# Kernel optimization log

Measured on AMD Instinct MI355X. Metric: run time of the kernel, lower is better.

The kernel has to match this reference:

```python
import jax, jax.numpy as jnp
import numpy as np

T, B, D, HID, L = 256, 64, 1024, 1024, 2


def setup_inputs() -> dict:
    key = jax.random.key(0)
    k1, k2, k3 = jax.random.split(key, 3)
    X = jax.random.normal(k1, (T, B, D), dtype=jnp.float32)
    # Stacked gate weights in order (i, f, o, c); xavier-like scale.
    Wx = jax.random.normal(k2, (L, 4 * HID, D), dtype=jnp.float32) * 0.03
    Wh = jax.random.normal(k3, (L, 4 * HID, HID), dtype=jnp.float32) * 0.03
    # Combined bias (Linear bias + b_gate); forget-gate bias initialized to 1.
    b = jnp.zeros((L, 4 * HID), dtype=jnp.float32).at[:, HID:2 * HID].set(1.0)
    return {"X": X, "Wx": Wx, "Wh": Wh, "b": b}


def reference(X, Wx, Wh, b):
    num_layers, H4, _ = Wx.shape
    Hd = H4 // 4
    Bsz = X.shape[1]
    H0 = jnp.zeros((num_layers, Bsz, Hd), X.dtype)
    C0 = jnp.zeros((num_layers, Bsz, Hd), X.dtype)

    def step(carry, x_t):
        H, C = carry
        x = x_t
        Hn, Cn = [], []
        for l in range(num_layers):  # small fixed layer count
            # fused gate GEMM: [B, 4H]
            g = x @ Wx[l].T + H[l] @ Wh[l].T + b[l]
            i_g, f_g, o_g, c_g = jnp.split(g, 4, axis=-1)
            c = jax.nn.sigmoid(f_g) * C[l] + jax.nn.sigmoid(i_g) * jnp.tanh(c_g)
            h = jax.nn.sigmoid(o_g) * jnp.tanh(c)
            Hn.append(h)
            Cn.append(c)
            x = h  # dropout is identity in eval mode
        return (jnp.stack(Hn), jnp.stack(Cn)), x

    (Hf, Cf), outputs = jax.lax.scan(step, (H0, C0), X)
    return outputs, Hf, Cf
```

## Files before the change

kernel.cpp:

```cpp
#include <hip/hip_runtime.h>
#include <cstdint>
#include <cstddef>

typedef __attribute__((ext_vector_type(8))) short short8;
typedef __attribute__((ext_vector_type(4))) float floatx4;
typedef unsigned short u16;
typedef unsigned long long u64;

#define NSTEP 256

__device__ __forceinline__ unsigned f2b_rne(float x) {
  unsigned u = __builtin_bit_cast(unsigned, x);
  return (u + 0x7fffu + ((u >> 16) & 1u)) >> 16;
}
__device__ __forceinline__ float b2f(u16 b) {
  unsigned u = ((unsigned)b) << 16;
  return __builtin_bit_cast(float, u);
}
__device__ __forceinline__ float sigf(float x) {
  x = fminf(fmaxf(x, -30.f), 30.f);
  return __builtin_amdgcn_rcpf(1.f + __expf(-x));
}
__device__ __forceinline__ float tanhf_fast(float x) {
  x = fminf(fmaxf(x, -15.f), 15.f);
  float e = __expf(2.f * x);
  return (e - 1.f) * __builtin_amdgcn_rcpf(e + 1.f);
}

__device__ __forceinline__ unsigned ald(const unsigned* p) {
  return __hip_atomic_load(p, __ATOMIC_RELAXED, __HIP_MEMORY_SCOPE_AGENT);
}
__device__ __forceinline__ void ast(unsigned* p, unsigned v) {
  __hip_atomic_store(p, v, __ATOMIC_RELAXED, __HIP_MEMORY_SCOPE_AGENT);
}

__global__ void init_kernel(unsigned* h0, unsigned* h1) {
  int i = blockIdx.x * blockDim.x + threadIdx.x;
  if (i < 32768) { h0[i] = 0; h1[i] = 0; }
}

__global__ void init2_kernel(unsigned* fl) {
  int i = blockIdx.x * blockDim.x + threadIdx.x;
  if (i < 1536) fl[i] = 0;
}

__global__ void cast_kernel(const float* __restrict__ in, u16* __restrict__ out, int n4) {
  int i = blockIdx.x * blockDim.x + threadIdx.x;
  int stride = gridDim.x * blockDim.x;
  for (; i < n4; i += stride) {
    float4 v = ((const float4*)in)[i];
    unsigned lo = f2b_rne(v.x) | (f2b_rne(v.y) << 16);
    unsigned hi = f2b_rne(v.z) | (f2b_rne(v.w) << 16);
    ((uint2*)out)[i] = make_uint2(lo, hi);
  }
}

__global__ __launch_bounds__(256) void gemm_nt(
    const u16* __restrict__ A, const u16* __restrict__ B, u16* __restrict__ C) {
  __shared__ u16 As[128 * 32];
  __shared__ u16 Bs[128 * 32];
  const int bid = blockIdx.x;
  const int m_blk = (bid >> 5) << 7;
  const int n_blk = (bid & 31) << 7;
  const int tid = threadIdx.x;
  const int wv = tid >> 6, lane = tid & 63;
  const int q = lane >> 4, n16 = lane & 15;
  const int m0w = (wv >> 1) << 6, n0w = (wv & 1) << 6;

  const floatx4 vzero = {0.f, 0.f, 0.f, 0.f};
  floatx4 acc[4][4];
#pragma unroll
  for (int mt = 0; mt < 4; ++mt)
#pragma unroll
    for (int nt = 0; nt < 4; ++nt) acc[mt][nt] = vzero;

  for (int k0 = 0; k0 < 1024; k0 += 32) {
#pragma unroll
    for (int i = 0; i < 2; ++i) {
      int s = i * 256 + tid;
      int r = s >> 2, kk = (s & 3) << 3;
      int m = m_blk + r, k = k0 + kk;
      size_t a_off = (size_t)m * 1024 + k;
      size_t b_off = (size_t)(n_blk + r) * 1024 + k;
      __builtin_amdgcn_global_load_lds(
          (const __attribute__((address_space(1))) unsigned int*)(A + a_off),
          (__attribute__((address_space(3))) unsigned int*)(As + (size_t)(i * 256 + wv * 64) * 8),
          16, 0, 0);
      __builtin_amdgcn_global_load_lds(
          (const __attribute__((address_space(1))) unsigned int*)(B + b_off),
          (__attribute__((address_space(3))) unsigned int*)(Bs + (size_t)(i * 256 + wv * 64) * 8),
          16, 0, 0);
    }
    __syncthreads();
    short8 af[4], bf[4];
#pragma unroll
    for (int mt = 0; mt < 4; ++mt)
      af[mt] = *(const short8*)(As + (m0w + mt * 16 + n16) * 32 + q * 8);
#pragma unroll
    for (int nt = 0; nt < 4; ++nt)
      bf[nt] = *(const short8*)(Bs + (n0w + nt * 16 + n16) * 32 + q * 8);
#pragma unroll
    for (int mt = 0; mt < 4; ++mt)
#pragma unroll
      for (int nt = 0; nt < 4; ++nt)
        acc[mt][nt] = __builtin_amdgcn_mfma_f32_16x16x32_bf16(af[mt], bf[nt], acc[mt][nt], 0, 0, 0);
    __syncthreads();
  }
#pragma unroll
  for (int mt = 0; mt < 4; ++mt)
#pragma unroll
    for (int nt = 0; nt < 4; ++nt)
#pragma unroll
      for (int r = 0; r < 4; ++r) {
        int m = m_blk + m0w + mt * 16 + q * 4 + r;
        int n = n_blk + n0w + nt * 16 + n16;
        C[(size_t)m * 4096 + n] = (u16)f2b_rne(acc[mt][nt][r]);
      }
}

#define GEMM_Q(HROW, W)                                                        \
  {                                                                            \
    short8 a_[8][4];                                                           \
    _Pragma("unroll")                                                          \
    for (int c_ = 0; c_ < 8; ++c_) {                                           \
      int k_ = kq0 + c_ * 32 + q * 8;                                          \
      const unsigned* base_ = (HROW) + (k_ >> 4) * 512 + ((k_ & 15) >> 1);     \
      _Pragma("unroll")                                                        \
      for (int m_ = 0; m_ < 4; ++m_)                                           \
        a_[c_][m_] = *(const short8*)(base_ + (m_ * 16 + n16) * 8);            \
    }                                                                          \
    _Pragma("unroll")                                                          \
    for (int c_ = 0; c_ < 8; ++c_)                                             \
      _Pragma("unroll")                                                        \
      for (int m_ = 0; m_ < 4; ++m_)                                           \
        asm volatile("" : "+v"(a_[c_][m_]));                                   \
    _Pragma("unroll")                                                          \
    for (int c_ = 0; c_ < 8; ++c_)                                             \
      _Pragma("unroll")                                                        \
      for (int m_ = 0; m_ < 4; ++m_)                                           \
        _Pragma("unroll")                                                      \
        for (int g_ = 0; g_ < 4; ++g_)                                         \
          acc[m_][g_] = __builtin_amdgcn_mfma_f32_16x16x32_bf16(a_[c_][m_], (W)[g_][c_], acc[m_][g_], 0, 0, 0); \
  }

#define REDUCE_TOT()                                                           \
  _Pragma("unroll")                                                            \
  for (int m_ = 0; m_ < 4; ++m_) {                                             \
    if (m_ != wv) {                                                            \
      int slot_ = (m_ - (m_ > wv ? 1 : 0)) * 4;                                \
      _Pragma("unroll")                                                        \
      for (int g_ = 0; g_ < 4; ++g_)                                           \
        *(floatx4*)&red[wv][slot_ + g_][lane * 4] = acc[m_][g_];               \
    }                                                                          \
  }                                                                            \
  __syncthreads();                                                             \
  _Pragma("unroll")                                                            \
  for (int g_ = 0; g_ < 4; ++g_) tot[g_] = acc[wv][g_];                        \
  _Pragma("unroll")                                                            \
  for (int w2_ = 0; w2_ < 4; ++w2_) {                                          \
    if (w2_ != wv) {                                                           \
      int slot_ = (wv - (wv > w2_ ? 1 : 0)) * 4;                               \
      _Pragma("unroll")                                                        \
      for (int g_ = 0; g_ < 4; ++g_)                                           \
        tot[g_] += *(const floatx4*)&red[w2_][slot_ + g_][lane * 4];           \
    }                                                                          \
  }

#define POLL1(FLA, TGTA)                                                       \
  if (wv == 0) {                                                               \
    int spins_ = 0;                                                            \
    for (;;) {                                                                 \
      unsigned va_ = ald((FLA) + lane * 8);                                    \
      if (__all((int)(va_ >= (TGTA)))) break;                                  \
      __builtin_amdgcn_s_sleep(1);                                             \
      if (++spins_ > (1 << 17)) break;                                         \
    }                                                                          \
  }
#define POLL2(FLA, TGTA, FLB, TGTB)                                            \
  if (wv == 0) {                                                               \
    int spins_ = 0;                                                            \
    for (;;) {                                                                 \
      unsigned va_ = ald((FLA) + lane * 8);                                    \
      unsigned vb_ = ald((FLB) + lane * 8);                                    \
      if (__all((int)((va_ >= (TGTA)) & (vb_ >= (TGTB))))) break;              \
      __builtin_amdgcn_s_sleep(1);                                             \
      if (++spins_ > (1 << 17)) break;                                         \
    }                                                                          \
  }

__global__ __launch_bounds__(256, 1) void lstm_fused(
    const u16* __restrict__ Wh0b,
    const u16* __restrict__ Wx1b,
    const u16* __restrict__ Wh1b,
    const u16* __restrict__ G,
    const float* __restrict__ bias,
    unsigned* H0u,
    unsigned* H1u,
    unsigned* G1u,
    unsigned* FL,
    float* __restrict__ outp,
    float* __restrict__ hf,
    float* __restrict__ cf) {
  __shared__ float red[4][12][256];
  const int tid = threadIdx.x;
  const int wv = tid >> 6;
  const int lane = tid & 63;
  const int q = lane >> 4;
  const int n16 = lane & 15;
  const int gid = blockIdx.x >> 6;
  const int jb = blockIdx.x & 63;
  const int jg = (jb << 4) + n16;
  const int kq0 = wv << 8;
  unsigned* fl0 = FL;
  unsigned* fl1 = FL + 512;
  unsigned* fl2 = FL + 1024;
  const floatx4 vzero = {0.f, 0.f, 0.f, 0.f};

  if (gid == 0) {
    short8 wf[4][8];
#pragma unroll
    for (int g = 0; g < 4; ++g)
#pragma unroll
      for (int c = 0; c < 8; ++c)
        wf[g][c] = *(const short8*)(Wh0b + (size_t)(g * 1024 + jg) * 1024 + kq0 + c * 32 + q * 8);
#pragma unroll
    for (int g = 0; g < 4; ++g)
#pragma unroll
      for (int c = 0; c < 8; ++c) asm volatile("" : "+v"(wf[g][c]));

    float bs[4];
#pragma unroll
    for (int g = 0; g < 4; ++g) bs[g] = bias[g * 1024 + jg];
    float cst[4] = {0.f, 0.f, 0.f, 0.f};

    float gf[4][4];
#pragma unroll
    for (int g = 0; g < 4; ++g)
#pragma unroll
      for (int r = 0; r < 4; ++r)
        gf[g][r] = b2f(G[(size_t)(wv * 16 + q * 4 + r) * 4096 + g * 1024 + jg]);

    for (int t = 0; t < NSTEP; ++t) {
      POLL1(fl0, (unsigned)t);
      __syncthreads();

      floatx4 acc[4][4];
#pragma unroll
      for (int m = 0; m < 4; ++m)
#pragma unroll
        for (int g = 0; g < 4; ++g) acc[m][g] = vzero;
      GEMM_Q(H0u + (size_t)t * 32768, wf);

      floatx4 tot[4];
      REDUCE_TOT();

      unsigned* hnext = H0u + (size_t)(t + 1) * 32768 + jb * 512;
      float hsv[4];
#pragma unroll
      for (int r = 0; r < 4; ++r) {
        float pi = tot[0][r] + gf[0][r] + bs[0];
        float pf = tot[1][r] + gf[1][r] + bs[1];
        float po = tot[2][r] + gf[2][r] + bs[2];
        float pc = tot[3][r] + gf[3][r] + bs[3];
        float cn = sigf(pf) * cst[r] + sigf(pi) * tanhf_fast(pc);
        float h = sigf(po) * tanhf_fast(cn);
        cst[r] = cn;
        hsv[r] = h;
        int brow = wv * 16 + q * 4 + r;
        unsigned hv = f2b_rne(h);
        unsigned pv = (unsigned)__shfl_xor((int)hv, 1);
        if (!(n16 & 1)) ast(hnext + brow * 8 + (n16 >> 1), hv | (pv << 16));
      }

      __syncthreads();
      if (tid == 0) ast(fl0 + jb * 8, (unsigned)(t + 1));

      if (t + 1 < NSTEP) {
#pragma unroll
        for (int g = 0; g < 4; ++g)
#pragma unroll
          for (int r = 0; r < 4; ++r)
            gf[g][r] = b2f(G[(size_t)((t + 1) * 64 + wv * 16 + q * 4 + r) * 4096 + g * 1024 + jg]);
      }
      if (t == NSTEP - 1) {
#pragma unroll
        for (int r = 0; r < 4; ++r) {
          int brow = wv * 16 + q * 4 + r;
          hf[brow * 1024 + jg] = hsv[r];
          cf[brow * 1024 + jg] = cst[r];
        }
      }
    }
  } else if (gid == 1) {
    short8 wf[4][8];
#pragma unroll
    for (int g = 0; g < 4; ++g)
#pragma unroll
      for (int c = 0; c < 8; ++c)
        wf[g][c] = *(const short8*)(Wx1b + (size_t)(g * 1024 + jg) * 1024 + kq0 + c * 32 + q * 8);
#pragma unroll
    for (int g = 0; g < 4; ++g)
#pragma unroll
      for (int c = 0; c < 8; ++c) asm volatile("" : "+v"(wf[g][c]));

    for (int t = 0; t < NSTEP; ++t) {
      unsigned tgtb = (t >= 8) ? (unsigned)(t - 7) : 0u;
      POLL2(fl0, (unsigned)(t + 1), fl1, tgtb);
      __syncthreads();

      floatx4 acc[4][4];
#pragma unroll
      for (int m = 0; m < 4; ++m)
#pragma unroll
        for (int g = 0; g < 4; ++g) acc[m][g] = vzero;
      GEMM_Q(H0u + (size_t)(t + 1) * 32768, wf);

      floatx4 tot[4];
      REDUCE_TOT();

      unsigned* g1o = G1u + (size_t)(t & 7) * 131072 + jb * 2048;
#pragma unroll
      for (int r = 0; r < 4; ++r) {
        int b = wv * 16 + q * 4 + r;
#pragma unroll
        for (int g = 0; g < 4; ++g) {
          unsigned v = f2b_rne(tot[g][r]);
          unsigned pv = (unsigned)__shfl_xor((int)v, 1);
          if (!(n16 & 1)) ast(g1o + g * 512 + b * 8 + (n16 >> 1), v | (pv << 16));
        }
      }

      __syncthreads();
      if (tid == 0) ast(fl2 + jb * 8, (unsigned)(t + 1));
    }
  } else {
    short8 wf[4][8];
#pragma unroll
    for (int g = 0; g < 4; ++g)
#pragma unroll
      for (int c = 0; c < 8; ++c)
        wf[g][c] = *(const short8*)(Wh1b + (size_t)(g * 1024 + jg) * 1024 + kq0 + c * 32 + q * 8);
#pragma unroll
    for (int g = 0; g < 4; ++g)
#pragma unroll
      for (int c = 0; c < 8; ++c) asm volatile("" : "+v"(wf[g][c]));

    float bs[4];
#pragma unroll
    for (int g = 0; g < 4; ++g) bs[g] = bias[4096 + g * 1024 + jg];
    float cst[4] = {0.f, 0.f, 0.f, 0.f};

    for (int t = 0; t < NSTEP; ++t) {
      POLL2(fl2, (unsigned)(t + 1), fl1, (unsigned)t);
      __syncthreads();

      const unsigned* g1i = G1u + (size_t)(t & 7) * 131072 + jb * 2048;
      float gf[4][4];
#pragma unroll
      for (int g = 0; g < 4; ++g)
#pragma unroll
        for (int r = 0; r < 4; ++r) {
          int b = wv * 16 + q * 4 + r;
          unsigned dw = ald(g1i + g * 512 + b * 8 + (n16 >> 1));
          gf[g][r] = b2f((u16)(dw >> (16 * (n16 & 1))));
        }

      floatx4 acc[4][4];
#pragma unroll
      for (int m = 0; m < 4; ++m)
#pragma unroll
        for (int g = 0; g < 4; ++g) acc[m][g] = vzero;
      GEMM_Q(H1u + (size_t)t * 32768, wf);

      floatx4 tot[4];
      REDUCE_TOT();

      unsigned* hnext = H1u + (size_t)(t + 1) * 32768 + jb * 512;
      float hsv[4];
#pragma unroll
      for (int r = 0; r < 4; ++r) {
        float pi = tot[0][r] + gf[0][r] + bs[0];
        float pf = tot[1][r] + gf[1][r] + bs[1];
        float po = tot[2][r] + gf[2][r] + bs[2];
        float pc = tot[3][r] + gf[3][r] + bs[3];
        float cn = sigf(pf) * cst[r] + sigf(pi) * tanhf_fast(pc);
        float h = sigf(po) * tanhf_fast(cn);
        cst[r] = cn;
        hsv[r] = h;
        int brow = wv * 16 + q * 4 + r;
        unsigned hv = f2b_rne(h);
        unsigned pv = (unsigned)__shfl_xor((int)hv, 1);
        if (!(n16 & 1)) ast(hnext + brow * 8 + (n16 >> 1), hv | (pv << 16));
      }

      __syncthreads();
      if (tid == 0) ast(fl1 + jb * 8, (unsigned)(t + 1));

#pragma unroll
      for (int r = 0; r < 4; ++r) {
        int brow = wv * 16 + q * 4 + r;
        outp[((size_t)t * 64 + brow) * 1024 + jg] = hsv[r];
      }
      if (t == NSTEP - 1) {
#pragma unroll
        for (int r = 0; r < 4; ++r) {
          int brow = wv * 16 + q * 4 + r;
          hf[65536 + brow * 1024 + jg] = hsv[r];
          cf[65536 + brow * 1024 + jg] = cst[r];
        }
      }
    }
  }
}

extern "C" void kernel_launch(void* const* d_in, const int* in_sizes, int n_in,
                              void* d_out, int out_size, void* d_ws, size_t ws_size,
                              hipStream_t stream) {
  const float* X  = (const float*)d_in[0];
  const float* Wx = (const float*)d_in[1];
  const float* Wh = (const float*)d_in[2];
  const float* b  = (const float*)d_in[3];
  float* out = (float*)d_out;

  char* ws = (char*)d_ws;
  u16* Xbf  = (u16*)(ws);
  unsigned* G1 = (unsigned*)(ws);
  unsigned* FL = (unsigned*)(ws + 8388608);
  u16* Wxbf = (u16*)(ws + 33554432);
  u16* Whbf = (u16*)(ws + 50331648);
  unsigned* H0 = (unsigned*)(ws + 67108864);
  unsigned* H1 = (unsigned*)(ws + 100794368);
  u16* G    = (u16*)(ws + 134479872);

  float* out_seq = out;
  float* Hf = out + 16777216;
  float* Cf = out + 16777216 + 131072;

  init_kernel<<<128, 256, 0, stream>>>(H0, H1);
  cast_kernel<<<2048, 256, 0, stream>>>(X, Xbf, 16777216 / 4);
  cast_kernel<<<2048, 256, 0, stream>>>(Wx, Wxbf, 8388608 / 4);
  cast_kernel<<<2048, 256, 0, stream>>>(Wh, Whbf, 8388608 / 4);

  gemm_nt<<<4096, 256, 0, stream>>>(Xbf, Wxbf, G);

  init2_kernel<<<6, 256, 0, stream>>>(FL);

  lstm_fused<<<192, 256, 0, stream>>>(Whbf, Wxbf + 4194304, Whbf + 4194304, G, b,
                                      H0, H1, G1, FL, out_seq, Hf, Cf);
}
```

Baseline: 1.904 ms.

## Fuse layer-0 input projection into persistent LSTM kernel as a producer group

Removes the standalone input-projection GEMM kernel. A new group of 64 persistent blocks holds Wx0 in registers and computes each timestep's layer-0 input gates into an 8-slot ring buffer, signalled through a new flag array. The layer-0 recurrent group now polls that flag and reads the gates from the ring. This overlaps the input GEMM with the recurrence and avoids a separate launch plus a large intermediate write, at the cost of 64 more resident blocks, extra flag polling, and a producer that could throttle the recurrence.

```diff
diff --git a/kernel.cpp b/kernel.cpp
--- a/kernel.cpp
+++ b/kernel.cpp
@@ -41,7 +41,7 @@
 
 __global__ void init2_kernel(unsigned* fl) {
   int i = blockIdx.x * blockDim.x + threadIdx.x;
-  if (i < 1536) fl[i] = 0;
+  if (i < 2048) fl[i] = 0;
 }
 
 __global__ void cast_kernel(const float* __restrict__ in, u16* __restrict__ out, int n4) {
@@ -55,69 +55,6 @@
   }
 }
 
-__global__ __launch_bounds__(256) void gemm_nt(
-    const u16* __restrict__ A, const u16* __restrict__ B, u16* __restrict__ C) {
-  __shared__ u16 As[128 * 32];
-  __shared__ u16 Bs[128 * 32];
-  const int bid = blockIdx.x;
-  const int m_blk = (bid >> 5) << 7;
-  const int n_blk = (bid & 31) << 7;
-  const int tid = threadIdx.x;
-  const int wv = tid >> 6, lane = tid & 63;
-  const int q = lane >> 4, n16 = lane & 15;
-  const int m0w = (wv >> 1) << 6, n0w = (wv & 1) << 6;
-
-  const floatx4 vzero = {0.f, 0.f, 0.f, 0.f};
-  floatx4 acc[4][4];
-#pragma unroll
-  for (int mt = 0; mt < 4; ++mt)
-#pragma unroll
-    for (int nt = 0; nt < 4; ++nt) acc[mt][nt] = vzero;
-
-  for (int k0 = 0; k0 < 1024; k0 += 32) {
-#pragma unroll
-    for (int i = 0; i < 2; ++i) {
-      int s = i * 256 + tid;
-      int r = s >> 2, kk = (s & 3) << 3;
-      int m = m_blk + r, k = k0 + kk;
-      size_t a_off = (size_t)m * 1024 + k;
-      size_t b_off = (size_t)(n_blk + r) * 1024 + k;
-      __builtin_amdgcn_global_load_lds(
-          (const __attribute__((address_space(1))) unsigned int*)(A + a_off),
-          (__attribute__((address_space(3))) unsigned int*)(As + (size_t)(i * 256 + wv * 64) * 8),
-          16, 0, 0);
-      __builtin_amdgcn_global_load_lds(
-          (const __attribute__((address_space(1))) unsigned int*)(B + b_off),
-          (__attribute__((address_space(3))) unsigned int*)(Bs + (size_t)(i * 256 + wv * 64) * 8),
-          16, 0, 0);
-    }
-    __syncthreads();
-    short8 af[4], bf[4];
-#pragma unroll
-    for (int mt = 0; mt < 4; ++mt)
-      af[mt] = *(const short8*)(As + (m0w + mt * 16 + n16) * 32 + q * 8);
-#pragma unroll
-    for (int nt = 0; nt < 4; ++nt)
-      bf[nt] = *(const short8*)(Bs + (n0w + nt * 16 + n16) * 32 + q * 8);
-#pragma unroll
-    for (int mt = 0; mt < 4; ++mt)
-#pragma unroll
-      for (int nt = 0; nt < 4; ++nt)
-        acc[mt][nt] = __builtin_amdgcn_mfma_f32_16x16x32_bf16(af[mt], bf[nt], acc[mt][nt], 0, 0, 0);
-    __syncthreads();
-  }
-#pragma unroll
-  for (int mt = 0; mt < 4; ++mt)
-#pragma unroll
-    for (int nt = 0; nt < 4; ++nt)
-#pragma unroll
-      for (int r = 0; r < 4; ++r) {
-        int m = m_blk + m0w + mt * 16 + q * 4 + r;
-        int n = n_blk + n0w + nt * 16 + n16;
-        C[(size_t)m * 4096 + n] = (u16)f2b_rne(acc[mt][nt][r]);
-      }
-}
-
 #define GEMM_Q(HROW, W)                                                        \
   {                                                                            \
     short8 a_[8][4];                                                           \
@@ -128,6 +65,30 @@
       _Pragma("unroll")                                                        \
       for (int m_ = 0; m_ < 4; ++m_)                                           \
         a_[c_][m_] = *(const short8*)(base_ + (m_ * 16 + n16) * 8);            \
+    }                                                                          \
+    _Pragma("unroll")                                                          \
+    for (int c_ = 0; c_ < 8; ++c_)                                             \
+      _Pragma("unroll")                                                        \
+      for (int m_ = 0; m_ < 4; ++m_)                                           \
+        asm volatile("" : "+v"(a_[c_][m_]));                                   \
+    _Pragma("unroll")                                                          \
+    for (int c_ = 0; c_ < 8; ++c_)                                             \
+      _Pragma("unroll")                                                        \
+      for (int m_ = 0; m_ < 4; ++m_)                                           \
+        _Pragma("unroll")                                                      \
+        for (int g_ = 0; g_ < 4; ++g_)                                         \
+          acc[m_][g_] = __builtin_amdgcn_mfma_f32_16x16x32_bf16(a_[c_][m_], (W)[g_][c_], acc[m_][g_], 0, 0, 0); \
+  }
+
+#define GEMM_QX(XROW, W)                                                       \
+  {                                                                            \
+    short8 a_[8][4];                                                           \
+    _Pragma("unroll")                                                          \
+    for (int c_ = 0; c_ < 8; ++c_) {                                           \
+      int k_ = kq0 + c_ * 32 + q * 8;                                          \
+      _Pragma("unroll")                                                        \
+      for (int m_ = 0; m_ < 4; ++m_)                                           \
+        a_[c_][m_] = *(const short8*)((XROW) + (size_t)(m_ * 16 + n16) * 1024 + k_); \
     }                                                                          \
     _Pragma("unroll")                                                          \
     for (int c_ = 0; c_ < 8; ++c_)                                             \
@@ -190,12 +151,14 @@
 
 __global__ __launch_bounds__(256, 1) void lstm_fused(
     const u16* __restrict__ Wh0b,
+    const u16* __restrict__ Wx0b,
     const u16* __restrict__ Wx1b,
     const u16* __restrict__ Wh1b,
-    const u16* __restrict__ G,
+    const u16* __restrict__ Xb,
     const float* __restrict__ bias,
     unsigned* H0u,
     unsigned* H1u,
+    unsigned* G0u,
     unsigned* G1u,
     unsigned* FL,
     float* __restrict__ outp,
@@ -214,6 +177,7 @@
   unsigned* fl0 = FL;
   unsigned* fl1 = FL + 512;
   unsigned* fl2 = FL + 1024;
+  unsigned* fl3 = FL + 1536;
   const floatx4 vzero = {0.f, 0.f, 0.f, 0.f};
 
   if (gid == 0) {
@@ -233,16 +197,20 @@
     for (int g = 0; g < 4; ++g) bs[g] = bias[g * 1024 + jg];
     float cst[4] = {0.f, 0.f, 0.f, 0.f};
 
-    float gf[4][4];
-#pragma unroll
-    for (int g = 0; g < 4; ++g)
-#pragma unroll
-      for (int r = 0; r < 4; ++r)
-        gf[g][r] = b2f(G[(size_t)(wv * 16 + q * 4 + r) * 4096 + g * 1024 + jg]);
-
     for (int t = 0; t < NSTEP; ++t) {
-      POLL1(fl0, (unsigned)t);
-      __syncthreads();
+      POLL2(fl0, (unsigned)t, fl3, (unsigned)(t + 1));
+      __syncthreads();
+
+      const unsigned* g0i = G0u + (size_t)(t & 7) * 131072 + jb * 2048;
+      float gf[4][4];
+#pragma unroll
+      for (int g = 0; g < 4; ++g)
+#pragma unroll
+        for (int r = 0; r < 4; ++r) {
+          int b = wv * 16 + q * 4 + r;
+          unsigned dw = ald(g0i + g * 512 + b * 8 + (n16 >> 1));
+          gf[g][r] = b2f((u16)(dw >> (16 * (n16 & 1))));
+        }
 
       floatx4 acc[4][4];
 #pragma unroll
@@ -275,13 +243,6 @@
       __syncthreads();
       if (tid == 0) ast(fl0 + jb * 8, (unsigned)(t + 1));
 
-      if (t + 1 < NSTEP) {
-#pragma unroll
-        for (int g = 0; g < 4; ++g)
-#pragma unroll
-          for (int r = 0; r < 4; ++r)
-            gf[g][r] = b2f(G[(size_t)((t + 1) * 64 + wv * 16 + q * 4 + r) * 4096 + g * 1024 + jg]);
-      }
       if (t == NSTEP - 1) {
 #pragma unroll
         for (int r = 0; r < 4; ++r) {
@@ -292,6 +253,48 @@
       }
     }
   } else if (gid == 1) {
+    short8 wf[4][8];
+#pragma unroll
+    for (int g = 0; g < 4; ++g)
+#pragma unroll
+      for (int c = 0; c < 8; ++c)
+        wf[g][c] = *(const short8*)(Wx0b + (size_t)(g * 1024 + jg) * 1024 + kq0 + c * 32 + q * 8);
+#pragma unroll
+    for (int g = 0; g < 4; ++g)
+#pragma unroll
+      for (int c = 0; c < 8; ++c) asm volatile("" : "+v"(wf[g][c]));
+
+    for (int t = 0; t < NSTEP; ++t) {
+      unsigned tgtb = (t >= 8) ? (unsigned)(t - 7) : 0u;
+      POLL1(fl0, tgtb);
+      __syncthreads();
+
+      floatx4 acc[4][4];
+#pragma unroll
+      for (int m = 0; m < 4; ++m)
+#pragma unroll
+        for (int g = 0; g < 4; ++g) acc[m][g] = vzero;
+      GEMM_QX(Xb + (size_t)t * 65536, wf);
+
+      floatx4 tot[4];
+      REDUCE_TOT();
+
+      unsigned* g0o = G0u + (size_t)(t & 7) * 131072 + jb * 2048;
+#pragma unroll
+      for (int r = 0; r < 4; ++r) {
+        int b = wv * 16 + q * 4 + r;
+#pragma unroll
+        for (int g = 0; g < 4; ++g) {
+          unsigned v = f2b_rne(tot[g][r]);
+          unsigned pv = (unsigned)__shfl_xor((int)v, 1);
+          if (!(n16 & 1)) ast(g0o + g * 512 + b * 8 + (n16 >> 1), v | (pv << 16));
+        }
+      }
+
+      __syncthreads();
+      if (tid == 0) ast(fl3 + jb * 8, (unsigned)(t + 1));
+    }
+  } else if (gid == 2) {
     short8 wf[4][8];
 #pragma unroll
     for (int g = 0; g < 4; ++g)
@@ -424,27 +427,24 @@
 
   char* ws = (char*)d_ws;
   u16* Xbf  = (u16*)(ws);
-  unsigned* G1 = (unsigned*)(ws);
-  unsigned* FL = (unsigned*)(ws + 8388608);
   u16* Wxbf = (u16*)(ws + 33554432);
   u16* Whbf = (u16*)(ws + 50331648);
   unsigned* H0 = (unsigned*)(ws + 67108864);
   unsigned* H1 = (unsigned*)(ws + 100794368);
-  u16* G    = (u16*)(ws + 134479872);
+  unsigned* G0 = (unsigned*)(ws + 134479872);
+  unsigned* G1 = (unsigned*)(ws + 138674176);
+  unsigned* FL = (unsigned*)(ws + 142868480);
 
   float* out_seq = out;
   float* Hf = out + 16777216;
   float* Cf = out + 16777216 + 131072;
 
   init_kernel<<<128, 256, 0, stream>>>(H0, H1);
+  init2_kernel<<<8, 256, 0, stream>>>(FL);
   cast_kernel<<<2048, 256, 0, stream>>>(X, Xbf, 16777216 / 4);
   cast_kernel<<<2048, 256, 0, stream>>>(Wx, Wxbf, 8388608 / 4);
   cast_kernel<<<2048, 256, 0, stream>>>(Wh, Whbf, 8388608 / 4);
 
-  gemm_nt<<<4096, 256, 0, stream>>>(Xbf, Wxbf, G);
-
-  init2_kernel<<<6, 256, 0, stream>>>(FL);
-
-  lstm_fused<<<192, 256, 0, stream>>>(Whbf, Wxbf + 4194304, Whbf + 4194304, G, b,
-                                      H0, H1, G1, FL, out_seq, Hf, Cf);
-}
+  lstm_fused<<<256, 256, 0, stream>>>(Whbf, Wxbf, Wxbf + 4194304, Whbf + 4194304,
+                                      Xbf, b, H0, H1, G0, G1, FL, out_seq, Hf, Cf);
+}
```

After: 2.356 ms. 1.24x slower.
